# Performance work log

Measured on AMD Instinct MI355X. Metric: run time of the kernel, lower is better.

Reference implementation:

```python
import jax, jax.numpy as jnp
import numpy as np

WINDOW = 512          # init window_size
OVERLAP = WINDOW // 4 # 128
FADE = OVERLAP // 2   # 64
ROPE_BASE = 10000.0


def _rope(x, pos):
    # x: (B,H,nw,W,D), pos: (nw,W) float
    D = x.shape[-1]
    inv_freq = 1.0 / (ROPE_BASE ** (jnp.arange(0, D, 2, dtype=jnp.float32) / D))
    ang = pos[..., None] * inv_freq                     # (nw,W,D/2)
    cos = jnp.concatenate([jnp.cos(ang), jnp.cos(ang)], -1)[None, None]  # (1,1,nw,W,D)
    sin = jnp.concatenate([jnp.sin(ang), jnp.sin(ang)], -1)[None, None]
    x1, x2 = x[..., : D // 2], x[..., D // 2 :]
    rot = jnp.concatenate([-x2, x1], -1)
    return x * cos + rot * sin


def setup_inputs() -> dict:
    key = jax.random.key(0)
    k1, k2, k3 = jax.random.split(key, 3)
    B, H, L, D = 2, 16, 8192, 64
    return {
        "query": jax.random.normal(k1, (B, H, L, D), jnp.float32),
        "key": jax.random.normal(k2, (B, H, L, D), jnp.float32),
        "value": jax.random.normal(k3, (B, H, L, D), jnp.float32),
        "position_ids": jnp.arange(L, dtype=jnp.int64),
    }


def reference(query, key, value, position_ids):
    B, H, L, D = query.shape
    nw = L // WINDOW
    qw = query.reshape(B, H, nw, WINDOW, D)
    kw = key.reshape(B, H, nw, WINDOW, D)
    vw = value.reshape(B, H, nw, WINDOW, D)
    pos = position_ids.reshape(nw, WINDOW).astype(jnp.float32)

    q = _rope(qw, pos)
    k = _rope(kw, pos)

    scores = jnp.einsum("bhnqd,bhnkd->bhnqk", q, k) / jnp.sqrt(jnp.float32(D))
    attn = jax.nn.softmax(scores, axis=-1)
    win_out = jnp.einsum("bhnqk,bhnkd->bhnqd", attn, vw)  # (B,H,nw,W,D)

    # overlap-fade blend weights per window (middle windows fade at edges;
    # first/last windows use full weight). out = win_out * w / (w + 1e-8).
    fade_in = jnp.linspace(0.0, 1.0, FADE)
    fade_out = jnp.linspace(1.0, 0.0, FADE)
    w_mid = jnp.concatenate([fade_in, jnp.ones(WINDOW - 2 * FADE), fade_out])
    w_edge = jnp.ones(WINDOW)
    idx = jnp.arange(nw)
    is_edge = (idx == 0) | (idx == nw - 1)
    w = jnp.where(is_edge[:, None], w_edge[None, :], w_mid[None, :])  # (nw,W)
    scale = (w / (w + 1e-8))[None, None, :, :, None]
    out = win_out * scale
    return out.reshape(B, H, L, D)
```

## Files before the change

### kernel.cpp

```cpp
#include <hip/hip_runtime.h>

typedef _Float16 half8 __attribute__((ext_vector_type(8)));
typedef _Float16 half4 __attribute__((ext_vector_type(4)));
typedef _Float16 half2v __attribute__((ext_vector_type(2)));
typedef float floatx4 __attribute__((ext_vector_type(4)));

#define MFMA_F16 __builtin_amdgcn_mfma_f32_16x16x32_f16
#define FREQ (-0.41524101186092f)

static __device__ __forceinline__ unsigned pack_f16(float a, float b) {
    half2v h; h.x = (_Float16)a; h.y = (_Float16)b;
    return __builtin_bit_cast(unsigned, h);
}

__global__ __launch_bounds__(256, 4) void swa8(
    const float* __restrict__ Q, const float* __restrict__ K,
    const float* __restrict__ V, const int* __restrict__ pid,
    float* __restrict__ Out)
{
    __shared__ __align__(16) _Float16 lq[64 * 72];
    __shared__ __align__(16) _Float16 lk[2][32 * 64];
    __shared__ __align__(16) _Float16 lvt[2][64 * 32];

    const int bid     = blockIdx.x;
    const int quarter = (bid >> 3) & 3;
    const int win     = (bid & 7) | ((bid >> 5) << 3);
    const int n = win & 15, bh = win >> 4;
    const long long winrow = (long long)bh * 8192 + n * 512;
    const long long qbase  = winrow + quarter * 128;
    const float* Qb = Q + qbase * 64;
    const float* Kb = K + winrow * 64;
    const float* Vb = V + winrow * 64;
    float* Ob = Out + qbase * 64;
    const int pidq = n * 512 + quarter * 128;
    const int pidk = n * 512;

    const int tid = threadIdx.x, lane = tid & 63, wv = tid >> 6;
    const int l15 = lane & 15, quad = (lane >> 4) & 3;
    const float CS = 0.125f * 1.44269504088896f;

    half8 qf[2][2];
    {
        const int rowl = tid >> 2;
        const int dq   = (tid & 3) * 8;
        float ifq[8];
        #pragma unroll
        for (int i = 0; i < 8; ++i) ifq[i] = __builtin_exp2f((float)(dq + i) * FREQ);
        for (int rnd = 0; rnd < 2; ++rnd) {
            const float* src = Qb + (rnd * 64 + rowl) * 64;
            float pos = (float)pid[pidq + rnd * 64 + rowl];
            float4 a0 = *(const float4*)(src + dq);
            float4 a1 = *(const float4*)(src + dq + 4);
            float4 b0 = *(const float4*)(src + 32 + dq);
            float4 b1 = *(const float4*)(src + 36 + dq);
            float lo[8] = {a0.x,a0.y,a0.z,a0.w,a1.x,a1.y,a1.z,a1.w};
            float hi[8] = {b0.x,b0.y,b0.z,b0.w,b1.x,b1.y,b1.z,b1.w};
            half8 wlo, whi;
            #pragma unroll
            for (int i = 0; i < 8; ++i) {
                float sn, cn;
                __sincosf(pos * ifq[i], &sn, &cn);
                wlo[i] = (_Float16)((lo[i] * cn - hi[i] * sn) * CS);
                whi[i] = (_Float16)((hi[i] * cn + lo[i] * sn) * CS);
            }
            if (rnd) __syncthreads();
            *(half8*)&lq[rowl * 72 + dq]      = wlo;
            *(half8*)&lq[rowl * 72 + 32 + dq] = whi;
            __syncthreads();
            if ((wv >> 1) == rnd) {
                const int rb = (wv & 1) * 32;
                #pragma unroll
                for (int rt = 0; rt < 2; ++rt) {
                    qf[rt][0] = *(const half8*)&lq[(rb + rt * 16 + l15) * 72 + quad * 8];
                    qf[rt][1] = *(const half8*)&lq[(rb + rt * 16 + l15) * 72 + 32 + quad * 8];
                }
            }
        }
    }

    floatx4 o[2][4], ol[2];
    #pragma unroll
    for (int rt = 0; rt < 2; ++rt) {
        ol[rt] = (floatx4){0.f, 0.f, 0.f, 0.f};
        #pragma unroll
        for (int vt = 0; vt < 4; ++vt) o[rt][vt] = (floatx4){0.f, 0.f, 0.f, 0.f};
    }
    half8 onesf;
    #pragma unroll
    for (int i = 0; i < 8; ++i) onesf[i] = (_Float16)1.0f;

    const int key = tid >> 3;
    const int d0  = (tid & 7) * 4;
    const int dv  = tid & 63;
    const int k8  = tid >> 6;
    float if4[4];
    #pragma unroll
    for (int i = 0; i < 4; ++i) if4[i] = __builtin_exp2f((float)(d0 + i) * FREQ);
    const int klo_addr = key * 64 + (((d0 >> 3) ^ (key & 7)) * 8) + (d0 & 7);
    const int khi_addr = key * 64 + ((((d0 >> 3) + 4) ^ (key & 7)) * 8) + (d0 & 7);
    int vst_addr[2];
    #pragma unroll
    for (int h = 0; h < 2; ++h) {
        int g = 2 * k8 + h;
        vst_addr[h] = dv * 32 + (((g & 3) ^ ((dv >> 1) & 3)) * 8) + ((g >> 2) * 4);
    }
    const int ksw0 = (quad ^ (l15 & 7)) * 8;
    const int ksw1 = ((quad + 4) ^ (l15 & 7)) * 8;
    const int vsw  = (quad ^ ((l15 >> 1) & 3)) * 8;

    float4 ka  = *(const float4*)(Kb + key * 64 + d0);
    float4 kb2 = *(const float4*)(Kb + key * 64 + 32 + d0);
    float vr[8];
    #pragma unroll
    for (int i = 0; i < 8; ++i) vr[i] = Vb[(k8 * 8 + i) * 64 + dv];
    int kp = pid[pidk + key];

    for (int kc = 0; kc < 16; ++kc) {
        const int cur = kc & 1;
        float kpos = (float)kp;
        half4 klo, khi;
        {
            float a[4] = {ka.x, ka.y, ka.z, ka.w};
            float b[4] = {kb2.x, kb2.y, kb2.z, kb2.w};
            #pragma unroll
            for (int i = 0; i < 4; ++i) {
                float sn, cn;
                __sincosf(kpos * if4[i], &sn, &cn);
                klo[i] = (_Float16)(a[i] * cn - b[i] * sn);
                khi[i] = (_Float16)(b[i] * cn + a[i] * sn);
            }
        }
        half4 vh0, vh1;
        #pragma unroll
        for (int i = 0; i < 4; ++i) { vh0[i] = (_Float16)vr[i]; vh1[i] = (_Float16)vr[4 + i]; }

        *(half4*)&lk[cur][klo_addr] = klo;
        *(half4*)&lk[cur][khi_addr] = khi;
        *(half4*)&lvt[cur][vst_addr[0]] = vh0;
        *(half4*)&lvt[cur][vst_addr[1]] = vh1;
        __syncthreads();

        if (kc < 15) {
            const float* kn = Kb + (kc + 1) * 2048;
            const float* vn = Vb + (kc + 1) * 2048;
            ka  = *(const float4*)(kn + key * 64 + d0);
            kb2 = *(const float4*)(kn + key * 64 + 32 + d0);
            #pragma unroll
            for (int i = 0; i < 8; ++i) vr[i] = vn[(k8 * 8 + i) * 64 + dv];
            kp = pid[pidk + (kc + 1) * 32 + key];
        }

        half8 kf00 = *(const half8*)&lk[cur][l15 * 64 + ksw0];
        half8 kf01 = *(const half8*)&lk[cur][l15 * 64 + ksw1];
        half8 kf10 = *(const half8*)&lk[cur][(16 + l15) * 64 + ksw0];
        half8 kf11 = *(const half8*)&lk[cur][(16 + l15) * 64 + ksw1];
        half8 vf[4];
        #pragma unroll
        for (int vt = 0; vt < 4; ++vt)
            vf[vt] = *(const half8*)&lvt[cur][(vt * 16 + l15) * 32 + vsw];

        __builtin_amdgcn_s_setprio(1);
        #pragma unroll
        for (int rt = 0; rt < 2; ++rt) {
            floatx4 s0 = {0.f,0.f,0.f,0.f}, s1 = {0.f,0.f,0.f,0.f};
            s0 = MFMA_F16(kf00, qf[rt][0], s0, 0, 0, 0);
            s0 = MFMA_F16(kf01, qf[rt][1], s0, 0, 0, 0);
            s1 = MFMA_F16(kf10, qf[rt][0], s1, 0, 0, 0);
            s1 = MFMA_F16(kf11, qf[rt][1], s1, 0, 0, 0);

            union { unsigned u[4]; half8 h; } pfu;
            pfu.u[0] = pack_f16(__builtin_exp2f(s0[0]), __builtin_exp2f(s0[1]));
            pfu.u[1] = pack_f16(__builtin_exp2f(s0[2]), __builtin_exp2f(s0[3]));
            pfu.u[2] = pack_f16(__builtin_exp2f(s1[0]), __builtin_exp2f(s1[1]));
            pfu.u[3] = pack_f16(__builtin_exp2f(s1[2]), __builtin_exp2f(s1[3]));
            half8 pf = pfu.h;

            ol[rt] = MFMA_F16(pf, onesf, ol[rt], 0, 0, 0);
            #pragma unroll
            for (int vt = 0; vt < 4; ++vt)
                o[rt][vt] = MFMA_F16(pf, vf[vt], o[rt][vt], 0, 0, 0);
        }
        __builtin_amdgcn_s_setprio(0);
    }

    #pragma unroll
    for (int rt = 0; rt < 2; ++rt) {
        #pragma unroll
        for (int r = 0; r < 4; ++r) {
            int rowl = wv * 32 + rt * 16 + quad * 4 + r;
            int j = quarter * 128 + rowl;
            float w;
            if (n == 0 || n == 15)  w = 1.0f;
            else if (j < 64)        w = (float)j * (1.0f / 63.0f);
            else if (j >= 448)      w = (float)(511 - j) * (1.0f / 63.0f);
            else                    w = 1.0f;
            float f = (w / (w + 1e-8f)) / ol[rt][r];
            #pragma unroll
            for (int vt = 0; vt < 4; ++vt)
                Ob[rowl * 64 + vt * 16 + l15] = o[rt][vt][r] * f;
        }
    }
}

extern "C" void kernel_launch(void* const* d_in, const int* in_sizes, int n_in,
                              void* d_out, int out_size, void* d_ws, size_t ws_size,
                              hipStream_t stream) {
    const float* q   = (const float*)d_in[0];
    const float* k   = (const float*)d_in[1];
    const float* v   = (const float*)d_in[2];
    const int*   pid = (const int*)d_in[3];
    float* out = (float*)d_out;
    (void)in_sizes; (void)n_in; (void)out_size; (void)d_ws; (void)ws_size;
    swa8<<<dim3(2048), dim3(256), 0, stream>>>(q, k, v, pid, out);
}
```

Before: 280.2 us.

## Use 512-thread blocks over half windows, hardware sincos, and VALU row sums

Each block now handles 256 query rows (half a window) with 8 waves instead of 128 rows with 4 waves. K/V staging is split into 64-key chunks, so the rotary and f16 conversion of K/V is done half as many times per window. The softmax denominator MFMA against a ones vector is replaced by per-lane VALU sums reduced with shuffles at the end. Rotary sin/cos now uses the hardware sin/cos instructions on a fract'd revolution argument, which may lose accuracy at large positions. The grid shrinks to 1024 blocks, which reduces parallel slack and adds per-block register and LDS pressure.

Measured after the change: 325.9 us. 16.3% more time.

```diff
diff --git a/kernel.cpp b/kernel.cpp
--- a/kernel.cpp
+++ b/kernel.cpp
@@ -7,32 +7,39 @@
 
 #define MFMA_F16 __builtin_amdgcn_mfma_f32_16x16x32_f16
 #define FREQ (-0.41524101186092f)
+#define INV2PI 0.15915494309189535f
 
 static __device__ __forceinline__ unsigned pack_f16(float a, float b) {
     half2v h; h.x = (_Float16)a; h.y = (_Float16)b;
     return __builtin_bit_cast(unsigned, h);
 }
 
-__global__ __launch_bounds__(256, 4) void swa8(
+static __device__ __forceinline__ void hw_sincos(float rev, float* sn, float* cn) {
+    float f = __builtin_amdgcn_fractf(rev);
+    *sn = __builtin_amdgcn_sinf(f);
+    *cn = __builtin_amdgcn_cosf(f);
+}
+
+__global__ __launch_bounds__(512, 4) void swa10(
     const float* __restrict__ Q, const float* __restrict__ K,
     const float* __restrict__ V, const int* __restrict__ pid,
     float* __restrict__ Out)
 {
-    __shared__ __align__(16) _Float16 lq[64 * 72];
-    __shared__ __align__(16) _Float16 lk[2][32 * 64];
-    __shared__ __align__(16) _Float16 lvt[2][64 * 32];
-
-    const int bid     = blockIdx.x;
-    const int quarter = (bid >> 3) & 3;
-    const int win     = (bid & 7) | ((bid >> 5) << 3);
+    __shared__ __align__(16) _Float16 lq[128 * 72];
+    __shared__ __align__(16) _Float16 lk[2][4096];
+    __shared__ __align__(16) _Float16 lvt[2][4096];
+
+    const int bid   = blockIdx.x;
+    const int half_ = (bid >> 3) & 1;
+    const int win   = (bid & 7) | ((bid >> 4) << 3);
     const int n = win & 15, bh = win >> 4;
     const long long winrow = (long long)bh * 8192 + n * 512;
-    const long long qbase  = winrow + quarter * 128;
+    const long long qbase  = winrow + half_ * 256;
     const float* Qb = Q + qbase * 64;
     const float* Kb = K + winrow * 64;
     const float* Vb = V + winrow * 64;
     float* Ob = Out + qbase * 64;
-    const int pidq = n * 512 + quarter * 128;
+    const int pidq = n * 512 + half_ * 256;
     const int pidk = n * 512;
 
     const int tid = threadIdx.x, lane = tid & 63, wv = tid >> 6;
@@ -45,10 +52,11 @@
         const int dq   = (tid & 3) * 8;
         float ifq[8];
         #pragma unroll
-        for (int i = 0; i < 8; ++i) ifq[i] = __builtin_exp2f((float)(dq + i) * FREQ);
+        for (int i = 0; i < 8; ++i)
+            ifq[i] = __builtin_exp2f((float)(dq + i) * FREQ) * INV2PI;
         for (int rnd = 0; rnd < 2; ++rnd) {
-            const float* src = Qb + (rnd * 64 + rowl) * 64;
-            float pos = (float)pid[pidq + rnd * 64 + rowl];
+            const float* src = Qb + (rnd * 128 + rowl) * 64;
+            float pos = (float)pid[pidq + rnd * 128 + rowl];
             float4 a0 = *(const float4*)(src + dq);
             float4 a1 = *(const float4*)(src + dq + 4);
             float4 b0 = *(const float4*)(src + 32 + dq);
@@ -59,7 +67,7 @@
             #pragma unroll
             for (int i = 0; i < 8; ++i) {
                 float sn, cn;
-                __sincosf(pos * ifq[i], &sn, &cn);
+                hw_sincos(pos * ifq[i], &sn, &cn);
                 wlo[i] = (_Float16)((lo[i] * cn - hi[i] * sn) * CS);
                 whi[i] = (_Float16)((hi[i] * cn + lo[i] * sn) * CS);
             }
@@ -67,8 +75,8 @@
             *(half8*)&lq[rowl * 72 + dq]      = wlo;
             *(half8*)&lq[rowl * 72 + 32 + dq] = whi;
             __syncthreads();
-            if ((wv >> 1) == rnd) {
-                const int rb = (wv & 1) * 32;
+            if ((wv >> 2) == rnd) {
+                const int rb = (wv & 3) * 32;
                 #pragma unroll
                 for (int rt = 0; rt < 2; ++rt) {
                     qf[rt][0] = *(const half8*)&lq[(rb + rt * 16 + l15) * 72 + quad * 8];
@@ -78,31 +86,29 @@
         }
     }
 
-    floatx4 o[2][4], ol[2];
-    #pragma unroll
-    for (int rt = 0; rt < 2; ++rt) {
-        ol[rt] = (floatx4){0.f, 0.f, 0.f, 0.f};
+    floatx4 o[2][4];
+    float olr[2] = {0.f, 0.f};
+    #pragma unroll
+    for (int rt = 0; rt < 2; ++rt)
         #pragma unroll
         for (int vt = 0; vt < 4; ++vt) o[rt][vt] = (floatx4){0.f, 0.f, 0.f, 0.f};
-    }
-    half8 onesf;
-    #pragma unroll
-    for (int i = 0; i < 8; ++i) onesf[i] = (_Float16)1.0f;
-
-    const int key = tid >> 3;
-    const int d0  = (tid & 7) * 4;
-    const int dv  = tid & 63;
-    const int k8  = tid >> 6;
+
+    const int key  = tid >> 3;
+    const int d0   = (tid & 7) * 4;
+    const int dv   = tid & 63;
+    const int kgrp = tid >> 6;
     float if4[4];
     #pragma unroll
-    for (int i = 0; i < 4; ++i) if4[i] = __builtin_exp2f((float)(d0 + i) * FREQ);
+    for (int i = 0; i < 4; ++i)
+        if4[i] = __builtin_exp2f((float)(d0 + i) * FREQ) * INV2PI;
     const int klo_addr = key * 64 + (((d0 >> 3) ^ (key & 7)) * 8) + (d0 & 7);
     const int khi_addr = key * 64 + ((((d0 >> 3) + 4) ^ (key & 7)) * 8) + (d0 & 7);
     int vst_addr[2];
     #pragma unroll
     for (int h = 0; h < 2; ++h) {
-        int g = 2 * k8 + h;
-        vst_addr[h] = dv * 32 + (((g & 3) ^ ((dv >> 1) & 3)) * 8) + ((g >> 2) * 4);
+        int g = 2 * kgrp + h;
+        vst_addr[h] = (g >> 3) * 2048 + dv * 32
+                    + (((g & 7) & 3) ^ ((dv >> 1) & 3)) * 8 + (((g & 7) >> 2) * 4);
     }
     const int ksw0 = (quad ^ (l15 & 7)) * 8;
     const int ksw1 = ((quad + 4) ^ (l15 & 7)) * 8;
@@ -112,10 +118,10 @@
     float4 kb2 = *(const float4*)(Kb + key * 64 + 32 + d0);
     float vr[8];
     #pragma unroll
-    for (int i = 0; i < 8; ++i) vr[i] = Vb[(k8 * 8 + i) * 64 + dv];
+    for (int i = 0; i < 8; ++i) vr[i] = Vb[(kgrp * 8 + i) * 64 + dv];
     int kp = pid[pidk + key];
 
-    for (int kc = 0; kc < 16; ++kc) {
+    for (int kc = 0; kc < 8; ++kc) {
         const int cur = kc & 1;
         float kpos = (float)kp;
         half4 klo, khi;
@@ -125,7 +131,7 @@
             #pragma unroll
             for (int i = 0; i < 4; ++i) {
                 float sn, cn;
-                __sincosf(kpos * if4[i], &sn, &cn);
+                hw_sincos(kpos * if4[i], &sn, &cn);
                 klo[i] = (_Float16)(a[i] * cn - b[i] * sn);
                 khi[i] = (_Float16)(b[i] * cn + a[i] * sn);
             }
@@ -140,61 +146,80 @@
         *(half4*)&lvt[cur][vst_addr[1]] = vh1;
         __syncthreads();
 
-        if (kc < 15) {
-            const float* kn = Kb + (kc + 1) * 2048;
-            const float* vn = Vb + (kc + 1) * 2048;
+        if (kc < 7) {
+            const float* kn = Kb + (kc + 1) * 4096;
+            const float* vn = Vb + (kc + 1) * 4096;
             ka  = *(const float4*)(kn + key * 64 + d0);
             kb2 = *(const float4*)(kn + key * 64 + 32 + d0);
             #pragma unroll
-            for (int i = 0; i < 8; ++i) vr[i] = vn[(k8 * 8 + i) * 64 + dv];
-            kp = pid[pidk + (kc + 1) * 32 + key];
-        }
-
-        half8 kf00 = *(const half8*)&lk[cur][l15 * 64 + ksw0];
-        half8 kf01 = *(const half8*)&lk[cur][l15 * 64 + ksw1];
-        half8 kf10 = *(const half8*)&lk[cur][(16 + l15) * 64 + ksw0];
-        half8 kf11 = *(const half8*)&lk[cur][(16 + l15) * 64 + ksw1];
-        half8 vf[4];
-        #pragma unroll
-        for (int vt = 0; vt < 4; ++vt)
-            vf[vt] = *(const half8*)&lvt[cur][(vt * 16 + l15) * 32 + vsw];
-
-        __builtin_amdgcn_s_setprio(1);
-        #pragma unroll
-        for (int rt = 0; rt < 2; ++rt) {
-            floatx4 s0 = {0.f,0.f,0.f,0.f}, s1 = {0.f,0.f,0.f,0.f};
-            s0 = MFMA_F16(kf00, qf[rt][0], s0, 0, 0, 0);
-            s0 = MFMA_F16(kf01, qf[rt][1], s0, 0, 0, 0);
-            s1 = MFMA_F16(kf10, qf[rt][0], s1, 0, 0, 0);
-            s1 = MFMA_F16(kf11, qf[rt][1], s1, 0, 0, 0);
-
-            union { unsigned u[4]; half8 h; } pfu;
-            pfu.u[0] = pack_f16(__builtin_exp2f(s0[0]), __builtin_exp2f(s0[1]));
-            pfu.u[1] = pack_f16(__builtin_exp2f(s0[2]), __builtin_exp2f(s0[3]));
-            pfu.u[2] = pack_f16(__builtin_exp2f(s1[0]), __builtin_exp2f(s1[1]));
-            pfu.u[3] = pack_f16(__builtin_exp2f(s1[2]), __builtin_exp2f(s1[3]));
-            half8 pf = pfu.h;
-
-            ol[rt] = MFMA_F16(pf, onesf, ol[rt], 0, 0, 0);
+            for (int i = 0; i < 8; ++i) vr[i] = vn[(kgrp * 8 + i) * 64 + dv];
+            kp = pid[pidk + (kc + 1) * 64 + key];
+        }
+
+        #pragma unroll
+        for (int s2 = 0; s2 < 2; ++s2) {
+            const _Float16* lkb = &lk[cur][s2 * 2048];
+            const _Float16* lvb = &lvt[cur][s2 * 2048];
+            half8 kf00 = *(const half8*)&lkb[l15 * 64 + ksw0];
+            half8 kf01 = *(const half8*)&lkb[l15 * 64 + ksw1];
+            half8 kf10 = *(const half8*)&lkb[(16 + l15) * 64 + ksw0];
+            half8 kf11 = *(const half8*)&lkb[(16 + l15) * 64 + ksw1];
+            half8 vf[4];
             #pragma unroll
             for (int vt = 0; vt < 4; ++vt)
-                o[rt][vt] = MFMA_F16(pf, vf[vt], o[rt][vt], 0, 0, 0);
-        }
-        __builtin_amdgcn_s_setprio(0);
-    }
-
+                vf[vt] = *(const half8*)&lvb[(vt * 16 + l15) * 32 + vsw];
+
+            __builtin_amdgcn_s_setprio(1);
+            #pragma unroll
+            for (int rt = 0; rt < 2; ++rt) {
+                floatx4 s0 = {0.f,0.f,0.f,0.f}, s1 = {0.f,0.f,0.f,0.f};
+                s0 = MFMA_F16(kf00, qf[rt][0], s0, 0, 0, 0);
+                s0 = MFMA_F16(kf01, qf[rt][1], s0, 0, 0, 0);
+                s1 = MFMA_F16(kf10, qf[rt][0], s1, 0, 0, 0);
+                s1 = MFMA_F16(kf11, qf[rt][1], s1, 0, 0, 0);
+
+                float p0 = __builtin_exp2f(s0[0]), p1 = __builtin_exp2f(s0[1]);
+                float p2 = __builtin_exp2f(s0[2]), p3 = __builtin_exp2f(s0[3]);
+                float p4 = __builtin_exp2f(s1[0]), p5 = __builtin_exp2f(s1[1]);
+                float p6 = __builtin_exp2f(s1[2]), p7 = __builtin_exp2f(s1[3]);
+                olr[rt] += ((p0 + p1) + (p2 + p3)) + ((p4 + p5) + (p6 + p7));
+
+                union { unsigned u[4]; half8 h; } pfu;
+                pfu.u[0] = pack_f16(p0, p1);
+                pfu.u[1] = pack_f16(p2, p3);
+                pfu.u[2] = pack_f16(p4, p5);
+                pfu.u[3] = pack_f16(p6, p7);
+                half8 pf = pfu.h;
+
+                #pragma unroll
+                for (int vt = 0; vt < 4; ++vt)
+                    o[rt][vt] = MFMA_F16(pf, vf[vt], o[rt][vt], 0, 0, 0);
+            }
+            __builtin_amdgcn_s_setprio(0);
+        }
+    }
+
+    float fullsum[2];
+    #pragma unroll
+    for (int rt = 0; rt < 2; ++rt) {
+        float v = olr[rt];
+        v += __shfl_xor(v, 16);
+        v += __shfl_xor(v, 32);
+        fullsum[rt] = v;
+    }
     #pragma unroll
     for (int rt = 0; rt < 2; ++rt) {
         #pragma unroll
         for (int r = 0; r < 4; ++r) {
             int rowl = wv * 32 + rt * 16 + quad * 4 + r;
-            int j = quarter * 128 + rowl;
+            float denom = __shfl(fullsum[rt], quad * 4 + r, 16);
+            int j = half_ * 256 + rowl;
             float w;
             if (n == 0 || n == 15)  w = 1.0f;
             else if (j < 64)        w = (float)j * (1.0f / 63.0f);
             else if (j >= 448)      w = (float)(511 - j) * (1.0f / 63.0f);
             else                    w = 1.0f;
-            float f = (w / (w + 1e-8f)) / ol[rt][r];
+            float f = (w / (w + 1e-8f)) / denom;
             #pragma unroll
             for (int vt = 0; vt < 4; ++vt)
                 Ob[rowl * 64 + vt * 16 + l15] = o[rt][vt][r] * f;
@@ -211,5 +236,5 @@
     const int*   pid = (const int*)d_in[3];
     float* out = (float*)d_out;
     (void)in_sizes; (void)n_in; (void)out_size; (void)d_ws; (void)ws_size;
-    swa8<<<dim3(2048), dim3(256), 0, stream>>>(q, k, v, pid, out);
-}
+    swa10<<<dim3(1024), dim3(512), 0, stream>>>(q, k, v, pid, out);
+}
```
